# Optimization experiments

Measured on AMD Instinct MI355X. Metric: run time of the kernel, lower is better.

## Reference

```python
import jax, jax.numpy as jnp
import numpy as np

NEG_SLOPE = 0.2

def _gat_layer(x, src, dst, W, a_s, a_d, b, concat):
    # x: [N, F_in], W: [F_in, H*C], a_s/a_d: [H, C]
    N = x.shape[0]
    H, C = a_s.shape
    h = (x @ W).reshape(N, H, C)                       # per-head projection
    al_s = jnp.sum(h * a_s, axis=-1)                   # [N, H]
    al_d = jnp.sum(h * a_d, axis=-1)                   # [N, H]
    e = jax.nn.leaky_relu(al_s[src] + al_d[dst], NEG_SLOPE)  # [E, H]
    # segment softmax over incoming edges of each dst node
    m = jax.ops.segment_max(e, dst, num_segments=N)    # [N, H]
    ex = jnp.exp(e - m[dst])
    denom = jax.ops.segment_sum(ex, dst, num_segments=N)
    alpha = ex / denom[dst]                            # [E, H]
    msg = h[src] * alpha[:, :, None]                   # [E, H, C]
    out = jax.ops.segment_sum(msg, dst, num_segments=N)  # [N, H, C]
    if concat:
        return out.reshape(N, H * C) + b
    return out.mean(axis=1) + b


def setup_inputs() -> dict:
    key = jax.random.key(0)
    ks = jax.random.split(key, 12)
    N, F_in, H, C1, LAT, E = 16384, 512, 4, 128, 64, 262144
    x = jax.random.normal(ks[0], (N, F_in), dtype=jnp.float32)
    edge_index = jax.random.randint(ks[1], (2, E), 0, N, dtype=jnp.int64)
    s = 0.05
    return {
        'x': x,
        'edge_index': edge_index,
        'W1': jax.random.normal(ks[2], (F_in, H * C1), dtype=jnp.float32) * s,
        'a_src1': jax.random.normal(ks[3], (H, C1), dtype=jnp.float32) * s,
        'a_dst1': jax.random.normal(ks[4], (H, C1), dtype=jnp.float32) * s,
        'b1': jax.random.normal(ks[5], (H * C1,), dtype=jnp.float32) * s,
        'W2': jax.random.normal(ks[6], (H * C1, H * LAT), dtype=jnp.float32) * s,
        'a_src2': jax.random.normal(ks[7], (H, LAT), dtype=jnp.float32) * s,
        'a_dst2': jax.random.normal(ks[8], (H, LAT), dtype=jnp.float32) * s,
        'b2': jax.random.normal(ks[9], (LAT,), dtype=jnp.float32) * s,
    }


def reference(x, edge_index, W1, a_src1, a_dst1, b1, W2, a_src2, a_dst2, b2):
    N = x.shape[0]
    # PyG GATConv default add_self_loops=True
    loop = jnp.arange(N, dtype=edge_index.dtype)
    src = jnp.concatenate([edge_index[0], loop])
    dst = jnp.concatenate([edge_index[1], loop])
    h = jax.nn.relu(_gat_layer(x, src, dst, W1, a_src1, a_dst1, b1, concat=True))
    out = _gat_layer(h, src, dst, W2, a_src2, a_dst2, b2, concat=False)
    return out
```

## Files before the change

### kernel.cpp

```cpp
#include <hip/hip_runtime.h>
#include <stdint.h>
#include <stddef.h>
#include <limits.h>

typedef __bf16 bf16;
typedef __bf16 bf16x4 __attribute__((ext_vector_type(4)));
typedef __bf16 bf16x8 __attribute__((ext_vector_type(8)));
typedef float  f32x4  __attribute__((ext_vector_type(4)));

#define CAP 128

static __device__ __forceinline__ float lrelu(float x) { return x > 0.f ? x : 0.2f * x; }
static __device__ __forceinline__ float san(float v) { return (fabsf(v) < 1e4f) ? v : 0.0f; }
static __device__ __forceinline__ float wexp(float e) { return __expf(fminf(e, 30.f)); }

static __device__ __forceinline__ void async_load16(const bf16* g, bf16* l) {
  __builtin_amdgcn_global_load_lds((const __attribute__((address_space(1))) void*)g,
                                   (__attribute__((address_space(3))) void*)l, 16, 0, 0);
}

static __device__ __forceinline__ void drain_barrier() {
  asm volatile("s_waitcnt vmcnt(0) lgkmcnt(0)" ::: "memory");
  __builtin_amdgcn_s_barrier();
}


__global__ __launch_bounds__(256) void prep_w(int* __restrict__ cnt,
                                              const float* __restrict__ W1,
                                              const float* __restrict__ W2,
                                              bf16* __restrict__ W1T,
                                              bf16* __restrict__ W2T,
                                              int N) {
  int b = blockIdx.x;
  if (b < N / 256) { cnt[b * 256 + threadIdx.x] = 0; return; }
  b -= N / 256;
  __shared__ bf16 t[32][33];
  const float* in; bf16* out; int R, C, bx, by;
  if (b < 256) { in = W1; out = W1T; R = 512; C = 512; by = b >> 4; bx = b & 15; }
  else         { b -= 256; in = W2; out = W2T; R = 512; C = 256; by = b >> 3; bx = b & 7; }
  const int lane = threadIdx.x & 31, r8 = threadIdx.x >> 5;
#pragma unroll
  for (int k = 0; k < 4; ++k) {
    int r = by * 32 + r8 + k * 8, c = bx * 32 + lane;
    t[lane][r8 + k * 8] = (bf16)san(in[(size_t)r * C + c]);
  }
  __syncthreads();
#pragma unroll
  for (int k = 0; k < 4; ++k) {
    int oc = bx * 32 + r8 + k * 8;
    out[(size_t)oc * R + by * 32 + lane] = t[r8 + k * 8][lane];
  }
}


__global__ __launch_bounds__(256) void gemm_al_l1(const float* __restrict__ X,
                                                  const bf16* __restrict__ BT,
                                                  bf16* __restrict__ C,
                                                  const float* __restrict__ a_s,
                                                  const float* __restrict__ a_d,
                                                  float* __restrict__ al_s,
                                                  float* __restrict__ al_d,
                                                  const int* __restrict__ src,
                                                  const int* __restrict__ dst,
                                                  int E, int* __restrict__ cnt,
                                                  int* __restrict__ slots,
                                                  int M, int N, int K) {
  __shared__ __align__(16) bf16 As[2][64 * 32];
  __shared__ __align__(16) bf16 Bs[2][128 * 32];
  __shared__ float alred[2][64][2];
  const int tid = threadIdx.x;
  const int b   = blockIdx.x;

  if (b >= 1024) {
    for (int e = (b - 1024) * 256 + tid; e < E; e += 256 * 256) {
      int d = dst[e];
      int pos = atomicAdd(&cnt[d], 1);
      if (pos < CAP) slots[(size_t)d * CAP + pos] = src[e];
    }
    return;
  }

  const int lane = tid & 63;
  const int wave = tid >> 6;
  const int m0 = (b & 255) * 64;
  const int head = b >> 8;
  const int n0 = head * 128;
  const int wm = (wave >> 1) * 32;
  const int wn = (wave & 1) * 64;

  f32x4 acc[2][4] = {};

  const int id1 = tid + 256;
  const float* apx = X  + (size_t)(m0 + (tid >> 2)) * K + (tid & 3) * 8;
  const bf16*  b0p = BT + (size_t)(n0 + (tid >> 2)) * K + (tid & 3) * 8;
  const bf16*  b1p = BT + (size_t)(n0 + (id1 >> 2)) * K + (id1 & 3) * 8;

  const int kq = (lane >> 4) * 8;
  const int rA = wm + (lane & 15);
  const int rB = wn + (lane & 15);

  {
    async_load16(b0p, &Bs[0][tid * 8]);
    async_load16(b1p, &Bs[0][id1 * 8]);
    f32x4 u0 = *(const f32x4*)(apx);
    f32x4 u1 = *(const f32x4*)(apx + 4);
    bf16x8 w;
#pragma unroll
    for (int k = 0; k < 4; ++k) { w[k] = (bf16)san(u0[k]); w[4 + k] = (bf16)san(u1[k]); }
    *(bf16x8*)&As[0][tid * 8] = w;
    drain_barrier();
  }

  int cur = 0;
  for (int k0 = 0; k0 < K; k0 += 32) {
    const int kn = (k0 + 32 < K) ? (k0 + 32) : k0;
    async_load16(b0p + kn, &Bs[cur ^ 1][tid * 8]);
    async_load16(b1p + kn, &Bs[cur ^ 1][id1 * 8]);
    f32x4 u0 = *(const f32x4*)(apx + kn);
    f32x4 u1 = *(const f32x4*)(apx + kn + 4);

    bf16x8 af[2], bfv[4];
#pragma unroll
    for (int i = 0; i < 2; ++i) af[i]  = *(const bf16x8*)&As[cur][(rA + i * 16) * 32 + kq];
#pragma unroll
    for (int j = 0; j < 4; ++j) bfv[j] = *(const bf16x8*)&Bs[cur][(rB + j * 16) * 32 + kq];
#pragma unroll
    for (int i = 0; i < 2; ++i)
#pragma unroll
      for (int j = 0; j < 4; ++j)
        acc[i][j] = __builtin_amdgcn_mfma_f32_16x16x32_bf16(af[i], bfv[j], acc[i][j], 0, 0, 0);

    bf16x8 w;
#pragma unroll
    for (int k = 0; k < 4; ++k) { w[k] = (bf16)san(u0[k]); w[4 + k] = (bf16)san(u1[k]); }
    *(bf16x8*)&As[cur ^ 1][tid * 8] = w;

    drain_barrier();
    cur ^= 1;
  }

  const int cc = lane & 15;
  const int rb = (lane >> 4) * 4;
#pragma unroll
  for (int i = 0; i < 2; ++i)
#pragma unroll
    for (int j = 0; j < 4; ++j) {
      int gcol = n0 + wn + j * 16 + cc;
#pragma unroll
      for (int r = 0; r < 4; ++r) {
        int grow = m0 + wm + i * 16 + rb + r;
        C[(size_t)grow * N + gcol] = (bf16)acc[i][j][r];
      }
    }

  {
    float asv[4], adv[4];
#pragma unroll
    for (int j = 0; j < 4; ++j) {
      int col = head * 128 + wn + j * 16 + cc;
      asv[j] = san(a_s[col]);
      adv[j] = san(a_d[col]);
    }
    const int wnh = wn >> 6;
#pragma unroll
    for (int i = 0; i < 2; ++i)
#pragma unroll
      for (int r = 0; r < 4; ++r) {
        float ps = 0.f, pd = 0.f;
#pragma unroll
        for (int j = 0; j < 4; ++j) { ps += acc[i][j][r] * asv[j]; pd += acc[i][j][r] * adv[j]; }
#pragma unroll
        for (int off = 1; off <= 8; off <<= 1) {
          ps += __shfl_xor(ps, off);
          pd += __shfl_xor(pd, off);
        }
        if (cc == 0) {
          int row = wm + i * 16 + rb + r;
          alred[wnh][row][0] = ps;
          alred[wnh][row][1] = pd;
        }
      }
    __syncthreads();
    if (tid < 64) {
      al_s[(size_t)(m0 + tid) * 4 + head] = alred[0][tid][0] + alred[1][tid][0];
      al_d[(size_t)(m0 + tid) * 4 + head] = alred[0][tid][1] + alred[1][tid][1];
    }
  }
}


__global__ __launch_bounds__(256) void gemm_al_l2(const bf16* __restrict__ A,
                                                  const bf16* __restrict__ BT,
                                                  bf16* __restrict__ C,
                                                  const float* __restrict__ a_s,
                                                  const float* __restrict__ a_d,
                                                  float* __restrict__ al_s,
                                                  float* __restrict__ al_d,
                                                  int M, int N, int K) {
  __shared__ __align__(16) bf16 As[2][64 * 32];
  __shared__ __align__(16) bf16 Bs[2][128 * 32];
  const int tid  = threadIdx.x;
  const int lane = tid & 63;
  const int wave = tid >> 6;
  const int m0 = blockIdx.x * 64;
  const int n0 = blockIdx.y * 128;
  const int wm = (wave >> 1) * 32;
  const int wn = (wave & 1) * 64;

  f32x4 acc[2][4] = {};

  const int tb = tid + 256;
  const bf16* ap  = A  + (size_t)(m0 + (tid >> 2)) * K + (tid & 3) * 8;
  const bf16* bp0 = BT + (size_t)(n0 + (tid >> 2)) * K + (tid & 3) * 8;
  const bf16* bp1 = BT + (size_t)(n0 + (tb  >> 2)) * K + (tb  & 3) * 8;

  const int kq = (lane >> 4) * 8;
  const int rA = wm + (lane & 15);
  const int rB = wn + (lane & 15);

  async_load16(ap,  &As[0][tid * 8]);
  async_load16(bp0, &Bs[0][tid * 8]);
  async_load16(bp1, &Bs[0][tb  * 8]);
  drain_barrier();

  int cur = 0;
  for (int k0 = 0; k0 < K; k0 += 32) {
    const int kn = (k0 + 32 < K) ? (k0 + 32) : k0;
    async_load16(ap  + kn, &As[cur ^ 1][tid * 8]);
    async_load16(bp0 + kn, &Bs[cur ^ 1][tid * 8]);
    async_load16(bp1 + kn, &Bs[cur ^ 1][tb  * 8]);

    bf16x8 af[2], bfv[4];
#pragma unroll
    for (int i = 0; i < 2; ++i) af[i]  = *(const bf16x8*)&As[cur][(rA + i * 16) * 32 + kq];
#pragma unroll
    for (int j = 0; j < 4; ++j) bfv[j] = *(const bf16x8*)&Bs[cur][(rB + j * 16) * 32 + kq];
#pragma unroll
    for (int i = 0; i < 2; ++i)
#pragma unroll
      for (int j = 0; j < 4; ++j)
        acc[i][j] = __builtin_amdgcn_mfma_f32_16x16x32_bf16(af[i], bfv[j], acc[i][j], 0, 0, 0);

    drain_barrier();
    cur ^= 1;
  }

  const int cc = lane & 15;
  const int rb = (lane >> 4) * 4;
#pragma unroll
  for (int i = 0; i < 2; ++i)
#pragma unroll
    for (int j = 0; j < 4; ++j) {
      int gcol = n0 + wn + j * 16 + cc;
#pragma unroll
      for (int r = 0; r < 4; ++r) {
        int grow = m0 + wm + i * 16 + rb + r;
        C[(size_t)grow * N + gcol] = (bf16)acc[i][j][r];
      }
    }

  {
    const int head = blockIdx.y * 2 + (wn >> 6);
    float asv[4], adv[4];
#pragma unroll
    for (int j = 0; j < 4; ++j) {
      int col = head * 64 + j * 16 + cc;
      asv[j] = san(a_s[col]);
      adv[j] = san(a_d[col]);
    }
#pragma unroll
    for (int i = 0; i < 2; ++i)
#pragma unroll
      for (int r = 0; r < 4; ++r) {
        float ps = 0.f, pd = 0.f;
#pragma unroll
        for (int j = 0; j < 4; ++j) { ps += acc[i][j][r] * asv[j]; pd += acc[i][j][r] * adv[j]; }
#pragma unroll
        for (int off = 1; off <= 8; off <<= 1) {
          ps += __shfl_xor(ps, off);
          pd += __shfl_xor(pd, off);
        }
        if (cc == 0) {
          int row = m0 + wm + i * 16 + rb + r;
          al_s[(size_t)row * 4 + head] = ps;
          al_d[(size_t)row * 4 + head] = pd;
        }
      }
  }
}


__global__ __launch_bounds__(256) void aggregate1_f(const bf16* __restrict__ h1,
                                                    const float* __restrict__ al_s,
                                                    const float* __restrict__ al_d,
                                                    const int* __restrict__ cnt,
                                                    int* __restrict__ slots,
                                                    const float* __restrict__ bias,
                                                    bf16* __restrict__ out) {
  __shared__ int   sIdx[4][64];
  __shared__ f32x4 sW[4][64];
  const int wv   = threadIdx.x >> 6;
  const int lane = threadIdx.x & 63;
  const int n = blockIdx.x * 4 + wv;
  const int cb = lane * 8;
  const int hd = lane >> 4;
  const int beg = n * CAP;
  const int len = min(cnt[n], CAP);
  const f32x4 alsn = *(const f32x4*)(al_s + (size_t)n * 4);
  const f32x4 aldn = *(const f32x4*)(al_d + (size_t)n * 4);

  const float wself = wexp(lrelu(alsn[hd] + aldn[hd]));
  bf16x8 hv0 = *(const bf16x8*)(h1 + (size_t)n * 512 + cb);
  float acc[8];
#pragma unroll
  for (int k = 0; k < 8; ++k) acc[k] = wself * (float)hv0[k];

  f32x4 Lv = {0.f, 0.f, 0.f, 0.f};
  if (lane == 0) {
#pragma unroll
    for (int h = 0; h < 4; ++h) Lv[h] = wexp(lrelu(alsn[h] + aldn[h]));
  }

  if (len <= 64) {
    int v = (lane < len) ? slots[beg + lane] : INT_MAX;
    if (len > 1) {
#pragma unroll
      for (int k = 2; k <= 64; k <<= 1) {
#pragma unroll
        for (int j = k >> 1; j > 0; j >>= 1) {
          int p = __shfl_xor(v, j);
          bool take_min = (((lane & k) == 0) == ((lane & j) == 0));
          v = take_min ? min(v, p) : max(v, p);
        }
      }
      if (lane < len) slots[beg + lane] = v;
    }
    if (lane < len) {
      sIdx[wv][lane] = v;
      f32x4 a = *(const f32x4*)(al_s + (size_t)v * 4);
      f32x4 w;
#pragma unroll
      for (int h = 0; h < 4; ++h) w[h] = wexp(lrelu(a[h] + aldn[h]));
      sW[wv][lane] = w;
#pragma unroll
      for (int h = 0; h < 4; ++h) Lv[h] += w[h];
    }
#pragma unroll 4
    for (int j = 0; j < len; ++j) {
      int s = sIdx[wv][j];
      float a = sW[wv][j][hd];
      bf16x8 hv = *(const bf16x8*)(h1 + (size_t)s * 512 + cb);
#pragma unroll
      for (int k = 0; k < 8; ++k) acc[k] += a * (float)hv[k];
    }
  } else {
    if (lane == 0) {
      for (int i = beg + 1; i < beg + len; ++i) {
        int v = slots[i];
        int j = i - 1;
        while (j >= beg && slots[j] > v) { slots[j + 1] = slots[j]; --j; }
        slots[j + 1] = v;
      }
    }
    asm volatile("s_waitcnt vmcnt(0)" ::: "memory");
    for (int c0 = beg; c0 < beg + len; c0 += 64) {
      const int cl = min(64, beg + len - c0);
      if (lane < cl) {
        int s = slots[c0 + lane];
        sIdx[wv][lane] = s;
        f32x4 a = *(const f32x4*)(al_s + (size_t)s * 4);
        f32x4 w;
#pragma unroll
        for (int h = 0; h < 4; ++h) w[h] = wexp(lrelu(a[h] + aldn[h]));
        sW[wv][lane] = w;
#pragma unroll
        for (int h = 0; h < 4; ++h) Lv[h] += w[h];
      }
#pragma unroll 4
      for (int j = 0; j < cl; ++j) {
        int s = sIdx[wv][j];
        float a = sW[wv][j][hd];
        bf16x8 hv = *(const bf16x8*)(h1 + (size_t)s * 512 + cb);
#pragma unroll
        for (int k = 0; k < 8; ++k) acc[k] += a * (float)hv[k];
      }
    }
  }

  for (int off = 32; off; off >>= 1) {
#pragma unroll
    for (int h = 0; h < 4; ++h) Lv[h] += __shfl_xor(Lv[h], off);
  }
  const float inv = 1.0f / Lv[hd];
  bf16x8 ov;
#pragma unroll
  for (int k = 0; k < 8; ++k)
    ov[k] = (bf16)fmaxf(acc[k] * inv + san(bias[cb + k]), 0.f);
  *(bf16x8*)(out + (size_t)n * 512 + cb) = ov;
}


__global__ __launch_bounds__(256) void aggregate2_f(const bf16* __restrict__ h2,
                                                    const float* __restrict__ al_s,
                                                    const float* __restrict__ al_d,
                                                    const int* __restrict__ cnt,
                                                    const int* __restrict__ slots,
                                                    const float* __restrict__ bias,
                                                    float* __restrict__ out) {
  __shared__ int   sIdx[4][64];
  __shared__ f32x4 sW[4][64];
  const int wv   = threadIdx.x >> 6;
  const int lane = threadIdx.x & 63;
  const int n = blockIdx.x * 4 + wv;
  const int hd = lane >> 4;
  const int cb = lane * 4;
  const int beg = n * CAP;
  const int len = min(cnt[n], CAP);
  const f32x4 alsn = *(const f32x4*)(al_s + (size_t)n * 4);
  const f32x4 aldn = *(const f32x4*)(al_d + (size_t)n * 4);

  const float wself = wexp(lrelu(alsn[hd] + aldn[hd]));
  bf16x4 hv0 = *(const bf16x4*)(h2 + (size_t)n * 256 + cb);
  float acc0 = wself * (float)hv0[0], acc1 = wself * (float)hv0[1];
  float acc2 = wself * (float)hv0[2], acc3 = wself * (float)hv0[3];
  f32x4 Lv = {0.f, 0.f, 0.f, 0.f};
  if (lane == 0) {
#pragma unroll
    for (int h = 0; h < 4; ++h) Lv[h] = wexp(lrelu(alsn[h] + aldn[h]));
  }
  for (int c0 = beg; c0 < beg + len; c0 += 64) {
    const int cl = min(64, beg + len - c0);
    if (lane < cl) {
      int s = slots[c0 + lane];
      sIdx[wv][lane] = s;
      f32x4 a = *(const f32x4*)(al_s + (size_t)s * 4);
      f32x4 w;
#pragma unroll
      for (int h = 0; h < 4; ++h) w[h] = wexp(lrelu(a[h] + aldn[h]));
      sW[wv][lane] = w;
#pragma unroll
      for (int h = 0; h < 4; ++h) Lv[h] += w[h];
    }
#pragma unroll 4
    for (int j = 0; j < cl; ++j) {
      int s = sIdx[wv][j];
      float a = sW[wv][j][hd];
      bf16x4 hv = *(const bf16x4*)(h2 + (size_t)s * 256 + cb);
      acc0 += a * (float)hv[0];
      acc1 += a * (float)hv[1];
      acc2 += a * (float)hv[2];
      acc3 += a * (float)hv[3];
    }
  }
  for (int off = 32; off; off >>= 1) {
#pragma unroll
    for (int h = 0; h < 4; ++h) Lv[h] += __shfl_xor(Lv[h], off);
  }
  const float inv = 1.0f / Lv[hd];
  acc0 *= inv; acc1 *= inv; acc2 *= inv; acc3 *= inv;
  acc0 += __shfl_xor(acc0, 16); acc1 += __shfl_xor(acc1, 16);
  acc2 += __shfl_xor(acc2, 16); acc3 += __shfl_xor(acc3, 16);
  acc0 += __shfl_xor(acc0, 32); acc1 += __shfl_xor(acc1, 32);
  acc2 += __shfl_xor(acc2, 32); acc3 += __shfl_xor(acc3, 32);
  if (lane < 16) {
    int ob = lane * 4;
    f32x4 ov;
    ov[0] = 0.25f * acc0 + san(bias[ob]);
    ov[1] = 0.25f * acc1 + san(bias[ob + 1]);
    ov[2] = 0.25f * acc2 + san(bias[ob + 2]);
    ov[3] = 0.25f * acc3 + san(bias[ob + 3]);
    *(f32x4*)(out + (size_t)n * 64 + ob) = ov;
  }
}


extern "C" void kernel_launch(void* const* d_in, const int* in_sizes, int n_in,
                              void* d_out, int out_size, void* d_ws, size_t ws_size,
                              hipStream_t stream) {
  const float* x   = (const float*)d_in[0];
  const int*   ei  = (const int*)d_in[1];
  const float* W1  = (const float*)d_in[2];
  const float* as1 = (const float*)d_in[3];
  const float* ad1 = (const float*)d_in[4];
  const float* b1  = (const float*)d_in[5];
  const float* W2  = (const float*)d_in[6];
  const float* as2 = (const float*)d_in[7];
  const float* ad2 = (const float*)d_in[8];
  const float* b2  = (const float*)d_in[9];
  float* outp = (float*)d_out;

  const int N = in_sizes[0] / 512;
  const int E = in_sizes[1] / 2;
  const int* src = ei;
  const int* dst = ei + E;

  char* p = (char*)d_ws;
  auto alloc = [&](size_t bytes) {
    char* r = p;
    p += (bytes + 255) & ~(size_t)255;
    return r;
  };
  bf16* h1    = (bf16*)alloc((size_t)N * 512 * 2);
  bf16* hbuf  = (bf16*)alloc((size_t)N * 512 * 2);
  bf16* W1T   = (bf16*)alloc((size_t)512 * 512 * 2);
  bf16* W2T   = (bf16*)alloc((size_t)256 * 512 * 2);
  float* al_s1 = (float*)alloc((size_t)N * 4 * 4);
  float* al_d1 = (float*)alloc((size_t)N * 4 * 4);
  float* al_s2 = (float*)alloc((size_t)N * 4 * 4);
  float* al_d2 = (float*)alloc((size_t)N * 4 * 4);
  int* cnt     = (int*)alloc((size_t)N * 4);
  int* slots   = (int*)alloc((size_t)N * CAP * 4);
  bf16* h2 = h1;

  prep_w<<<N / 256 + 256 + 128, 256, 0, stream>>>(cnt, W1, W2, W1T, W2T, N);

  gemm_al_l1<<<1024 + 256, 256, 0, stream>>>(x, W1T, h1, as1, ad1, al_s1, al_d1,
                                             src, dst, E, cnt, slots, N, 512, 512);
  aggregate1_f<<<N / 4, 256, 0, stream>>>(h1, al_s1, al_d1, cnt, slots, b1, hbuf);

  gemm_al_l2<<<dim3(N / 64, 2), 256, 0, stream>>>(hbuf, W2T, h2, as2, ad2, al_s2, al_d2,
                                                  N, 256, 512);
  aggregate2_f<<<N / 4, 256, 0, stream>>>(h2, al_s2, al_d2, cnt, slots, b2, outp);
}
```

Measured before the change: 188.9 us.

## Batch gather loads in aggregation, shrink layer-2 GEMM tiles, widen edge binning

The aggregation kernels now issue eight independent row gathers before accumulating, instead of one load per dependent iteration, to raise memory-level parallelism; tail slots are clamped and weighted zero. The layer-2 GEMM switches to 64x64 tiles with one head per block, doubling the grid and reducing attention logits through shared memory. Edge binning in the layer-1 GEMM launch gets twice as many blocks, and the fp32 A loads are issued before the async B loads. The costs are more registers in aggregation, wasted clamped loads on short neighbor lists, and more redundant A-tile reads in the layer-2 GEMM.

```diff
diff --git a/kernel.cpp b/kernel.cpp
--- a/kernel.cpp
+++ b/kernel.cpp
@@ -72,7 +72,7 @@
   const int b   = blockIdx.x;
 
   if (b >= 1024) {
-    for (int e = (b - 1024) * 256 + tid; e < E; e += 256 * 256) {
+    for (int e = (b - 1024) * 256 + tid; e < E; e += 512 * 256) {
       int d = dst[e];
       int pos = atomicAdd(&cnt[d], 1);
       if (pos < CAP) slots[(size_t)d * CAP + pos] = src[e];
@@ -100,10 +100,10 @@
   const int rB = wn + (lane & 15);
 
   {
+    f32x4 u0 = *(const f32x4*)(apx);
+    f32x4 u1 = *(const f32x4*)(apx + 4);
     async_load16(b0p, &Bs[0][tid * 8]);
     async_load16(b1p, &Bs[0][id1 * 8]);
-    f32x4 u0 = *(const f32x4*)(apx);
-    f32x4 u1 = *(const f32x4*)(apx + 4);
     bf16x8 w;
 #pragma unroll
     for (int k = 0; k < 4; ++k) { w[k] = (bf16)san(u0[k]); w[4 + k] = (bf16)san(u1[k]); }
@@ -114,10 +114,10 @@
   int cur = 0;
   for (int k0 = 0; k0 < K; k0 += 32) {
     const int kn = (k0 + 32 < K) ? (k0 + 32) : k0;
+    f32x4 u0 = *(const f32x4*)(apx + kn);
+    f32x4 u1 = *(const f32x4*)(apx + kn + 4);
     async_load16(b0p + kn, &Bs[cur ^ 1][tid * 8]);
     async_load16(b1p + kn, &Bs[cur ^ 1][id1 * 8]);
-    f32x4 u0 = *(const f32x4*)(apx + kn);
-    f32x4 u1 = *(const f32x4*)(apx + kn + 4);
 
     bf16x8 af[2], bfv[4];
 #pragma unroll
@@ -198,47 +198,45 @@
                                                   float* __restrict__ al_d,
                                                   int M, int N, int K) {
   __shared__ __align__(16) bf16 As[2][64 * 32];
-  __shared__ __align__(16) bf16 Bs[2][128 * 32];
+  __shared__ __align__(16) bf16 Bs[2][64 * 32];
+  __shared__ float alred[2][64][2];
   const int tid  = threadIdx.x;
   const int lane = tid & 63;
   const int wave = tid >> 6;
-  const int m0 = blockIdx.x * 64;
-  const int n0 = blockIdx.y * 128;
+  const int m0   = blockIdx.x * 64;
+  const int head = blockIdx.y;
+  const int n0   = head * 64;
   const int wm = (wave >> 1) * 32;
-  const int wn = (wave & 1) * 64;
-
-  f32x4 acc[2][4] = {};
-
-  const int tb = tid + 256;
-  const bf16* ap  = A  + (size_t)(m0 + (tid >> 2)) * K + (tid & 3) * 8;
-  const bf16* bp0 = BT + (size_t)(n0 + (tid >> 2)) * K + (tid & 3) * 8;
-  const bf16* bp1 = BT + (size_t)(n0 + (tb  >> 2)) * K + (tb  & 3) * 8;
+  const int wn = (wave & 1) * 32;
+
+  f32x4 acc[2][2] = {};
+
+  const bf16* ap = A  + (size_t)(m0 + (tid >> 2)) * K + (tid & 3) * 8;
+  const bf16* bp = BT + (size_t)(n0 + (tid >> 2)) * K + (tid & 3) * 8;
 
   const int kq = (lane >> 4) * 8;
   const int rA = wm + (lane & 15);
   const int rB = wn + (lane & 15);
 
-  async_load16(ap,  &As[0][tid * 8]);
-  async_load16(bp0, &Bs[0][tid * 8]);
-  async_load16(bp1, &Bs[0][tb  * 8]);
+  async_load16(ap, &As[0][tid * 8]);
+  async_load16(bp, &Bs[0][tid * 8]);
   drain_barrier();
 
   int cur = 0;
   for (int k0 = 0; k0 < K; k0 += 32) {
     const int kn = (k0 + 32 < K) ? (k0 + 32) : k0;
-    async_load16(ap  + kn, &As[cur ^ 1][tid * 8]);
-    async_load16(bp0 + kn, &Bs[cur ^ 1][tid * 8]);
-    async_load16(bp1 + kn, &Bs[cur ^ 1][tb  * 8]);
-
-    bf16x8 af[2], bfv[4];
+    async_load16(ap + kn, &As[cur ^ 1][tid * 8]);
+    async_load16(bp + kn, &Bs[cur ^ 1][tid * 8]);
+
+    bf16x8 af[2], bfv[2];
 #pragma unroll
     for (int i = 0; i < 2; ++i) af[i]  = *(const bf16x8*)&As[cur][(rA + i * 16) * 32 + kq];
 #pragma unroll
-    for (int j = 0; j < 4; ++j) bfv[j] = *(const bf16x8*)&Bs[cur][(rB + j * 16) * 32 + kq];
+    for (int j = 0; j < 2; ++j) bfv[j] = *(const bf16x8*)&Bs[cur][(rB + j * 16) * 32 + kq];
 #pragma unroll
     for (int i = 0; i < 2; ++i)
 #pragma unroll
-      for (int j = 0; j < 4; ++j)
+      for (int j = 0; j < 2; ++j)
         acc[i][j] = __builtin_amdgcn_mfma_f32_16x16x32_bf16(af[i], bfv[j], acc[i][j], 0, 0, 0);
 
     drain_barrier();
@@ -250,7 +248,7 @@
 #pragma unroll
   for (int i = 0; i < 2; ++i)
 #pragma unroll
-    for (int j = 0; j < 4; ++j) {
+    for (int j = 0; j < 2; ++j) {
       int gcol = n0 + wn + j * 16 + cc;
 #pragma unroll
       for (int r = 0; r < 4; ++r) {
@@ -260,32 +258,37 @@
     }
 
   {
-    const int head = blockIdx.y * 2 + (wn >> 6);
-    float asv[4], adv[4];
-#pragma unroll
-    for (int j = 0; j < 4; ++j) {
-      int col = head * 64 + j * 16 + cc;
+    float asv[2], adv[2];
+#pragma unroll
+    for (int j = 0; j < 2; ++j) {
+      int col = n0 + wn + j * 16 + cc;
       asv[j] = san(a_s[col]);
       adv[j] = san(a_d[col]);
     }
+    const int wnh = wn >> 5;
 #pragma unroll
     for (int i = 0; i < 2; ++i)
 #pragma unroll
       for (int r = 0; r < 4; ++r) {
         float ps = 0.f, pd = 0.f;
 #pragma unroll
-        for (int j = 0; j < 4; ++j) { ps += acc[i][j][r] * asv[j]; pd += acc[i][j][r] * adv[j]; }
+        for (int j = 0; j < 2; ++j) { ps += acc[i][j][r] * asv[j]; pd += acc[i][j][r] * adv[j]; }
 #pragma unroll
         for (int off = 1; off <= 8; off <<= 1) {
           ps += __shfl_xor(ps, off);
           pd += __shfl_xor(pd, off);
         }
         if (cc == 0) {
-          int row = m0 + wm + i * 16 + rb + r;
-          al_s[(size_t)row * 4 + head] = ps;
-          al_d[(size_t)row * 4 + head] = pd;
+          int row = wm + i * 16 + rb + r;
+          alred[wnh][row][0] = ps;
+          alred[wnh][row][1] = pd;
         }
       }
+    __syncthreads();
+    if (tid < 64) {
+      al_s[(size_t)(m0 + tid) * 4 + head] = alred[0][tid][0] + alred[1][tid][0];
+      al_d[(size_t)(m0 + tid) * 4 + head] = alred[0][tid][1] + alred[1][tid][1];
+    }
   }
 }
 
@@ -345,13 +348,20 @@
 #pragma unroll
       for (int h = 0; h < 4; ++h) Lv[h] += w[h];
     }
-#pragma unroll 4
-    for (int j = 0; j < len; ++j) {
-      int s = sIdx[wv][j];
-      float a = sW[wv][j][hd];
-      bf16x8 hv = *(const bf16x8*)(h1 + (size_t)s * 512 + cb);
-#pragma unroll
-      for (int k = 0; k < 8; ++k) acc[k] += a * (float)hv[k];
+    for (int j0 = 0; j0 < len; j0 += 8) {
+      bf16x8 rv[8];
+      float  wt[8];
+#pragma unroll
+      for (int t = 0; t < 8; ++t) {
+        int jj = j0 + t;
+        int s  = sIdx[wv][jj < len ? jj : len - 1];
+        rv[t]  = *(const bf16x8*)(h1 + (size_t)s * 512 + cb);
+        wt[t]  = (jj < len) ? sW[wv][jj][hd] : 0.f;
+      }
+#pragma unroll
+      for (int t = 0; t < 8; ++t)
+#pragma unroll
+        for (int k = 0; k < 8; ++k) acc[k] += wt[t] * (float)rv[t][k];
     }
   } else {
     if (lane == 0) {
@@ -376,13 +386,20 @@
 #pragma unroll
         for (int h = 0; h < 4; ++h) Lv[h] += w[h];
       }
-#pragma unroll 4
-      for (int j = 0; j < cl; ++j) {
-        int s = sIdx[wv][j];
-        float a = sW[wv][j][hd];
-        bf16x8 hv = *(const bf16x8*)(h1 + (size_t)s * 512 + cb);
-#pragma unroll
-        for (int k = 0; k < 8; ++k) acc[k] += a * (float)hv[k];
+      for (int j0 = 0; j0 < cl; j0 += 8) {
+        bf16x8 rv[8];
+        float  wt[8];
+#pragma unroll
+        for (int t = 0; t < 8; ++t) {
+          int jj = j0 + t;
+          int s  = sIdx[wv][jj < cl ? jj : cl - 1];
+          rv[t]  = *(const bf16x8*)(h1 + (size_t)s * 512 + cb);
+          wt[t]  = (jj < cl) ? sW[wv][jj][hd] : 0.f;
+        }
+#pragma unroll
+        for (int t = 0; t < 8; ++t)
+#pragma unroll
+          for (int k = 0; k < 8; ++k) acc[k] += wt[t] * (float)rv[t][k];
       }
     }
   }
@@ -441,15 +458,23 @@
 #pragma unroll
       for (int h = 0; h < 4; ++h) Lv[h] += w[h];
     }
-#pragma unroll 4
-    for (int j = 0; j < cl; ++j) {
-      int s = sIdx[wv][j];
-      float a = sW[wv][j][hd];
-      bf16x4 hv = *(const bf16x4*)(h2 + (size_t)s * 256 + cb);
-      acc0 += a * (float)hv[0];
-      acc1 += a * (float)hv[1];
-      acc2 += a * (float)hv[2];
-      acc3 += a * (float)hv[3];
+    for (int j0 = 0; j0 < cl; j0 += 8) {
+      bf16x4 rv[8];
+      float  wt[8];
+#pragma unroll
+      for (int t = 0; t < 8; ++t) {
+        int jj = j0 + t;
+        int s  = sIdx[wv][jj < cl ? jj : cl - 1];
+        rv[t]  = *(const bf16x4*)(h2 + (size_t)s * 256 + cb);
+        wt[t]  = (jj < cl) ? sW[wv][jj][hd] : 0.f;
+      }
+#pragma unroll
+      for (int t = 0; t < 8; ++t) {
+        acc0 += wt[t] * (float)rv[t][0];
+        acc1 += wt[t] * (float)rv[t][1];
+        acc2 += wt[t] * (float)rv[t][2];
+        acc3 += wt[t] * (float)rv[t][3];
+      }
     }
   }
   for (int off = 32; off; off >>= 1) {
@@ -514,11 +539,11 @@
 
   prep_w<<<N / 256 + 256 + 128, 256, 0, stream>>>(cnt, W1, W2, W1T, W2T, N);
 
-  gemm_al_l1<<<1024 + 256, 256, 0, stream>>>(x, W1T, h1, as1, ad1, al_s1, al_d1,
+  gemm_al_l1<<<1024 + 512, 256, 0, stream>>>(x, W1T, h1, as1, ad1, al_s1, al_d1,
                                              src, dst, E, cnt, slots, N, 512, 512);
   aggregate1_f<<<N / 4, 256, 0, stream>>>(h1, al_s1, al_d1, cnt, slots, b1, hbuf);
 
-  gemm_al_l2<<<dim3(N / 64, 2), 256, 0, stream>>>(hbuf, W2T, h2, as2, ad2, al_s2, al_d2,
+  gemm_al_l2<<<dim3(N / 64, 4), 256, 0, stream>>>(hbuf, W2T, h2, as2, ad2, al_s2, al_d2,
                                                   N, 256, 512);
   aggregate2_f<<<N / 4, 256, 0, stream>>>(h2, al_s2, al_d2, cnt, slots, b2, outp);
 }
```

Result: slower. 193.6 us (+2.5%).
